# Kernel tuning notes

Hardware: AMD Instinct MI355X
Metric: run time of the kernel (lower is better)

## Reference

```python
import jax, jax.numpy as jnp
import numpy as np

# --- low precision float format: exp=5, man=2, subnormals, nearest-even ---
EXP, MAN = 5, 2
BIAS = 2 ** (EXP - 1) - 1          # 15
EMIN = 1 - BIAS                     # -14 (min normal exponent; clamping here gives subnormals)
MAXV = (2.0 - 2.0 ** (-MAN)) * 2.0 ** BIAS


def _q(x):
    """Round x to nearest FP(exp=5, man=2) value (subnormals, clipped at max)."""
    ax = jnp.abs(x)
    e = jnp.floor(jnp.log2(jnp.where(ax > 0, ax, 1.0)))
    e = jnp.maximum(e, EMIN)
    scale = jnp.exp2(e - MAN)
    q = jnp.round(x / scale) * scale   # jnp.round = half-to-even
    q = jnp.clip(q, -MAXV, MAXV)
    return jnp.where(ax > 0, q, x).astype(x.dtype)


# Quantizer: forward quantize, straight-through (quantized) backward
@jax.custom_vjp
def fq(x):
    return _q(x)

def _fq_fwd(x):
    return _q(x), None

def _fq_bwd(_, g):
    return (_q(g),)

fq.defvjp(_fq_fwd, _fq_bwd)


def conv_valid(x, w):
    return jax.lax.conv_general_dilated(
        x, w, window_strides=(1, 1), padding='VALID',
        dimension_numbers=('NCHW', 'OIHW', 'NCHW'))


def qconv(x, w):
    # QConv2d: input_quant, weight_quant, conv, output_quant
    return fq(conv_valid(fq(x), fq(w)))


def qlinear(x, W, b):
    # QLinear: input_quant, weight_quant (weights + bias), matmul, output_quant
    return fq(fq(x) @ fq(W).T + fq(b))


def batchnorm(x, gamma, beta, eps=1e-5):
    # training-mode BatchNorm2d over (N,H,W) per channel
    m = x.mean(axis=(0, 2, 3), keepdims=True)
    v = x.var(axis=(0, 2, 3), keepdims=True)
    return (x - m) * jax.lax.rsqrt(v + eps) * gamma[None, :, None, None] + beta[None, :, None, None]


def maxpool2(x):
    return jax.lax.reduce_window(x, -jnp.inf, jax.lax.max,
                                 (1, 1, 2, 2), (1, 1, 2, 2), 'VALID')


def setup_inputs() -> dict:
    key = jax.random.key(0)
    ks = jax.random.split(key, 12)
    B = 8192
    inp = {
        'x':   jax.random.normal(ks[0], (B, 1, 32, 32), jnp.float32),
        'w1':  jax.random.normal(ks[1], (6, 1, 5, 5), jnp.float32) * 0.2,
        'g1':  jnp.ones((6,), jnp.float32),
        'be1': jnp.zeros((6,), jnp.float32),
        'w2':  jax.random.normal(ks[2], (16, 6, 5, 5), jnp.float32) * 0.1,
        'g2':  jnp.ones((16,), jnp.float32),
        'be2': jnp.zeros((16,), jnp.float32),
        'fw1': jax.random.normal(ks[3], (120, 400), jnp.float32) * 0.05,
        'fb1': jnp.zeros((120,), jnp.float32),
        'fw2': jax.random.normal(ks[4], (84, 120), jnp.float32) * 0.09,
        'fb2': jnp.zeros((84,), jnp.float32),
        'fw3': jax.random.normal(ks[5], (10, 84), jnp.float32) * 0.1,
        'fb3': jnp.zeros((10,), jnp.float32),
    }
    return inp


def reference(x, w1, g1, be1, w2, g2, be2, fw1, fb1, fw2, fb2, fw3, fb3):
    x = fq(x)                                   # act_error_quant
    x = qconv(x, w1)                            # conv1 (no bias)
    x = batchnorm(x, g1, be1)                   # bn1
    x = fq(x)                                   # act_error_quant
    x = maxpool2(jax.nn.relu(x))                # relu + 2x2 maxpool -> [B,6,14,14]
    x = qconv(x, w2)                            # conv2 -> [B,16,10,10]
    x = batchnorm(x, g2, be2)                   # bn2
    x = fq(x)
    x = maxpool2(jax.nn.relu(x))                # -> [B,16,5,5]
    x = x.reshape(x.shape[0], -1)               # [B,400]
    x = jax.nn.relu(qlinear(x, fw1, fb1))       # fc1
    x = jax.nn.relu(qlinear(x, fw2, fb2))       # fc2
    x = qlinear(x, fw3, fb3)                    # fc3 -> [B,10]
    return x
```

## Files before the change

kernel.cpp:

```cpp
#include <hip/hip_runtime.h>
#include <hip/hip_bf16.h>


#define BATCH 8192

typedef double d4 __attribute__((ext_vector_type(4)));

__device__ __forceinline__ double fq_d(double x) {
    long long b = __double_as_longlong(x);
    long long ab = b & 0x7fffffffffffffffLL;
    if (ab == 0) return x;
    double q;
    if (ab >= 0x3F10000000000000LL) {
        long long r = b + 0x0001FFFFFFFFFFFFLL + ((b >> 50) & 1LL);
        r &= 0xFFFC000000000000LL;
        q = __longlong_as_double(r);
        q = fmin(fmax(q, -57344.0), 57344.0);
    } else {
        q = rint(x * 65536.0) * 1.52587890625e-05;
    }
    return q;
}

__device__ __forceinline__ float fq_f(float x) {
    int b = __float_as_int(x);
    int ab = b & 0x7fffffff;
    if (ab == 0) return x;
    float q;
    if (ab >= 0x38800000) {
        int r = b + 0x000FFFFF + ((b >> 21) & 1);
        r &= 0xFFE00000;
        q = __int_as_float(r);
        q = fminf(fmaxf(q, -57344.0f), 57344.0f);
    } else {
        q = rintf(x * 65536.0f) * 1.52587890625e-05f;
    }
    return q;
}

__device__ __forceinline__ unsigned short bfbits(double q) {
    __hip_bfloat16 h = __float2bfloat16((float)q);
    return *(unsigned short*)&h;
}

__global__ void kprep(const float* __restrict__ w1, const float* __restrict__ w2,
                      const float* __restrict__ fb1, const float* __restrict__ fb2,
                      const float* __restrict__ fb3, const float* __restrict__ fw1,
                      const float* __restrict__ fw2, const float* __restrict__ fw3,
                      float* __restrict__ qw1, float* __restrict__ qw2,
                      float* __restrict__ qfb1, float* __restrict__ qfb2,
                      float* __restrict__ qfb3, float* __restrict__ Wt1,
                      float* __restrict__ Wt2, float* __restrict__ Wt3) {
    int i = blockIdx.x * 256 + threadIdx.x;
    if (i < 150) { qw1[i] = fq_f(w1[i]); return; }
    i -= 150;
    if (i < 2400) { qw2[i] = fq_f(w2[i]); return; }
    i -= 2400;
    if (i < 120) { qfb1[i] = fq_f(fb1[i]); return; }
    i -= 120;
    if (i < 84) { qfb2[i] = fq_f(fb2[i]); return; }
    i -= 84;
    if (i < 10) { qfb3[i] = fq_f(fb3[i]); return; }
    i -= 10;
    if (i < 51200) { int k = i / 128, o = i % 128;
        Wt1[i] = (o < 120) ? fq_f(fw1[o * 400 + k]) : 0.0f; return; }
    i -= 51200;
    if (i < 15360) { int k = i / 128, o = i % 128;
        Wt2[i] = (o < 84) ? fq_f(fw2[o * 120 + k]) : 0.0f; return; }
    i -= 15360;
    if (i < 1344) { int k = i / 16, o = i % 16;
        Wt3[i] = (o < 10) ? fq_f(fw3[o * 84 + k]) : 0.0f; return; }
}
#define PREP_TOTAL (150 + 2400 + 120 + 84 + 10 + 51200 + 15360 + 1344)

__global__ __launch_bounds__(256) void kconv1(const float* __restrict__ x,
        const float* __restrict__ qw, __hip_bfloat16* __restrict__ c1,
        int nimg_total, double* __restrict__ st1) {
    __shared__ float sxf[3 * 1056];
    __shared__ double swd[152];
    __shared__ double sred[6][2];
    int t = threadIdx.x;
    int b0 = blockIdx.x * 3;
    int nimg = nimg_total - b0; if (nimg > 3) nimg = 3;
    for (int i = t; i < nimg * 1024; i += 256) {
        int img = i >> 10, idx = i & 1023;
        sxf[img * 1056 + (idx >> 5) * 33 + (idx & 31)] =
            fq_f(x[(size_t)(b0 + img) * 1024 + idx]);
    }
    if (t < 150) swd[t] = (double)qw[t];
    if (t >= 192 && t < 204) ((double*)sred)[t - 192] = 0.0;
    __syncthreads();
    int ntask = nimg * 336;
    for (int task = t; task < ntask; task += 256) {
        int img = task / 336; int rr = task % 336;
        int co = rr / 56; int rem = rr % 56;
        int i0 = (rem >> 2) * 2;
        int j0 = (rem & 3) * 7;
        const double* wp = &swd[co * 25];
        double a0[7], a1[7];
        #pragma unroll
        for (int j = 0; j < 7; ++j) { a0[j] = 0.0; a1[j] = 0.0; }
        double wr[5], wq[5];
        #pragma unroll
        for (int u = 0; u < 6; ++u) {
            const float* xr = &sxf[img * 1056 + (i0 + u) * 33 + j0];
            double xv[11];
            #pragma unroll
            for (int k = 0; k < 11; ++k) xv[k] = (double)xr[k];
            if (u < 5) {
                #pragma unroll
                for (int tt = 0; tt < 5; ++tt) wr[tt] = wp[u * 5 + tt];
                #pragma unroll
                for (int j = 0; j < 7; ++j)
                    a0[j] = fma(xv[j], wr[0], fma(xv[j+1], wr[1], fma(xv[j+2], wr[2],
                            fma(xv[j+3], wr[3], fma(xv[j+4], wr[4], a0[j])))));
            }
            if (u >= 1) {
                #pragma unroll
                for (int j = 0; j < 7; ++j)
                    a1[j] = fma(xv[j], wq[0], fma(xv[j+1], wq[1], fma(xv[j+2], wq[2],
                            fma(xv[j+3], wq[3], fma(xv[j+4], wq[4], a1[j])))));
            }
            #pragma unroll
            for (int tt = 0; tt < 5; ++tt) wq[tt] = wr[tt];
        }
        size_t base = ((size_t)(b0 + img) * 6 + co) * 784 + (size_t)i0 * 28 + j0;
        double s = 0.0, s2 = 0.0;
        #pragma unroll
        for (int j = 0; j < 7; ++j) {
            double q0 = fq_d(a0[j]), q1 = fq_d(a1[j]);
            ((unsigned short*)c1)[base + j]      = bfbits(q0);
            ((unsigned short*)c1)[base + 28 + j] = bfbits(q1);
            s += q0 + q1; s2 += q0 * q0 + q1 * q1;
        }
        atomicAdd(&sred[co][0], s);
        atomicAdd(&sred[co][1], s2);
    }
    __syncthreads();
    if (t < 12) atomicAdd(&st1[t * 32 + (blockIdx.x & 31)], ((double*)sred)[t]);
}

__global__ void kfinal(const double* __restrict__ st, double* __restrict__ mr,
                       int C, double N) {
    int c = threadIdx.x;
    if (c < C) {
        double s = 0.0, s2 = 0.0;
        for (int b = 0; b < 32; ++b) { s += st[c * 64 + b]; s2 += st[c * 64 + 32 + b]; }
        double m = s / N;
        double v = s2 / N - m * m;
        mr[2 * c] = m;
        mr[2 * c + 1] = 1.0 / sqrt(v + 1e-5);
    }
}

__global__ __launch_bounds__(256) void kpool1(const __hip_bfloat16* __restrict__ c1,
        const double* __restrict__ mr1, const float* __restrict__ g1,
        const float* __restrict__ be1, __hip_bfloat16* __restrict__ p1) {
    int idx = blockIdx.x * 256 + threadIdx.x;
    int pp = idx % 7;  int t1 = idx / 7;
    int ph = t1 % 14;  int t2 = t1 / 14;
    int c  = t2 % 6;   int b  = t2 / 6;
    double m = mr1[2 * c], r = mr1[2 * c + 1];
    double gg = (double)g1[c], bb = (double)be1[c];
    bool useMax = (r * gg) >= 0.0;
    const __hip_bfloat16* src = c1 + (((size_t)b * 6 + c) * 28 + 2 * ph) * 28 + 4 * pp;
    ushort4 u0 = *(const ushort4*)src;
    ushort4 u1 = *(const ushort4*)(src + 28);
    float f0 = __bfloat162float(*(__hip_bfloat16*)&u0.x), f1 = __bfloat162float(*(__hip_bfloat16*)&u0.y);
    float f2 = __bfloat162float(*(__hip_bfloat16*)&u0.z), f3 = __bfloat162float(*(__hip_bfloat16*)&u0.w);
    float f4 = __bfloat162float(*(__hip_bfloat16*)&u1.x), f5 = __bfloat162float(*(__hip_bfloat16*)&u1.y);
    float f6 = __bfloat162float(*(__hip_bfloat16*)&u1.z), f7 = __bfloat162float(*(__hip_bfloat16*)&u1.w);
    float va = useMax ? fmaxf(fmaxf(f0, f1), fmaxf(f4, f5))
                      : fminf(fminf(f0, f1), fminf(f4, f5));
    float vb = useMax ? fmaxf(fmaxf(f2, f3), fmaxf(f6, f7))
                      : fminf(fminf(f2, f3), fminf(f6, f7));
    double qa = fq_d((((double)va - m) * r) * gg + bb);
    double qb = fq_d((((double)vb - m) * r) * gg + bb);
    qa = fmax(qa, 0.0); qb = fmax(qb, 0.0);
    ushort2 pk; pk.x = bfbits(qa); pk.y = bfbits(qb);
    *(ushort2*)&p1[((size_t)b * 6 + c) * 196 + ph * 14 + 2 * pp] = pk;
}

__global__ __launch_bounds__(320) void kconv2(const __hip_bfloat16* __restrict__ p1,
        const float* __restrict__ qw, __hip_bfloat16* __restrict__ c2,
        double* __restrict__ st2) {
    __shared__ float sxf[9408];
    __shared__ double swd[2432];
    __shared__ int soff[152];
    __shared__ double sred[16][2];
    int t = threadIdx.x;
    int b0 = blockIdx.x * 8;
    const ushort4* srcp = (const ushort4*)(p1 + (size_t)b0 * 1176);
    for (int i = t; i < 2352; i += 320) {
        ushort4 u = srcp[i];
        float* d = &sxf[4 * i];
        d[0] = __bfloat162float(*(__hip_bfloat16*)&u.x);
        d[1] = __bfloat162float(*(__hip_bfloat16*)&u.y);
        d[2] = __bfloat162float(*(__hip_bfloat16*)&u.z);
        d[3] = __bfloat162float(*(__hip_bfloat16*)&u.w);
    }
    for (int i = t; i < 2432; i += 320) {
        int k = i >> 4, co = i & 15;
        swd[i] = (k < 150) ? (double)qw[co * 150 + k] : 0.0;
    }
    if (t < 152) {
        int k = t;
        soff[k] = (k < 150) ? (k / 25) * 196 + ((k % 25) / 5) * 14 + (k % 5) : 0;
    }
    if (t < 32) ((double*)sred)[t] = 0.0;
    __syncthreads();

    int l = t & 63, w = t >> 6;
    int c = l >> 4, r16 = l & 15;

    d4 pz = {0.0, 0.0, 0.0, 0.0};
    d4 prow = __builtin_amdgcn_mfma_f64_16x16x4f64((double)r16, 0.25, pz, 0, 0, 0);
    d4 pcol = __builtin_amdgcn_mfma_f64_16x16x4f64(1.0, 0.25 * (double)r16, pz, 0, 0, 0);
    int rowidx[4], colidx[4];
    #pragma unroll
    for (int j = 0; j < 4; ++j) { rowidx[j] = (int)prow[j]; colidx[j] = (int)pcol[j]; }

    double bw[38];
    #pragma unroll
    for (int s = 0; s < 38; ++s) bw[s] = swd[(4 * s + c) * 16 + r16];

    double ls = 0.0, ls2 = 0.0;
    int co0 = colidx[0];
    for (int tile = w; tile < 50; tile += 5) {
        int pos = tile * 16 + r16;
        int img = pos / 100, pp = pos % 100;
        int abase = img * 1176 + (pp / 10) * 14 + (pp % 10);
        d4 acc = {0.0, 0.0, 0.0, 0.0};
        #pragma unroll
        for (int s = 0; s < 38; ++s) {
            double av = (double)sxf[abase + soff[4 * s + c]];
            acc = __builtin_amdgcn_mfma_f64_16x16x4f64(av, bw[s], acc, 0, 0, 0);
        }
        #pragma unroll
        for (int j = 0; j < 4; ++j) {
            int po = tile * 16 + rowidx[j];
            int im2 = po / 100, pq = po % 100;
            double q = fq_d(acc[j]);
            ((unsigned short*)c2)[((size_t)(b0 + im2) * 100 + pq) * 16 + colidx[j]] = bfbits(q);
            ls += q; ls2 += q * q;
        }
    }
    atomicAdd(&sred[co0][0], ls);
    atomicAdd(&sred[co0][1], ls2);
    __syncthreads();
    if (t < 32) atomicAdd(&st2[t * 32 + (blockIdx.x & 31)], ((double*)sred)[t]);
}

__global__ __launch_bounds__(256) void kfc1(const __hip_bfloat16* __restrict__ c2,
        const double* __restrict__ st2, const float* __restrict__ g2,
        const float* __restrict__ be2, const float* __restrict__ Wt,
        const float* __restrict__ qb, __hip_bfloat16* __restrict__ outb) {
    constexpr int IN = 400, OUT = 120, OUTP = 128, ROWS = 4, BT = 8;
    __shared__ double sx[BT][IN];
    __shared__ double sbn[16][4];
    int t = threadIdx.x;
    int b0 = blockIdx.x * BT;
    if (t < 16) {
        double s = 0.0, s2 = 0.0;
        for (int b = 0; b < 32; ++b) { s += st2[t * 64 + b]; s2 += st2[t * 64 + 32 + b]; }
        double m = s / (819200.0);
        double v = s2 / (819200.0) - m * m;
        sbn[t][0] = m; sbn[t][1] = 1.0 / sqrt(v + 1e-5);
        sbn[t][2] = (double)g2[t]; sbn[t][3] = (double)be2[t];
    }
    __syncthreads();
    for (int i = t; i < BT * IN; i += 256) {
        int r = i / IN, k = i % IN;
        int c = k / 25, rem = k % 25;
        int ph = rem / 5, pw = rem % 5;
        const __hip_bfloat16* src = c2 + ((size_t)(b0 + r) * 100 + 20 * ph + 2 * pw) * 16 + c;
        double m = sbn[c][0], rr = sbn[c][1], gg = sbn[c][2], bb = sbn[c][3];
        float f0 = __bfloat162float(src[0]),   f1 = __bfloat162float(src[16]);
        float f2 = __bfloat162float(src[160]), f3 = __bfloat162float(src[176]);
        bool useMax = (rr * gg) >= 0.0;
        float v = useMax ? fmaxf(fmaxf(f0, f1), fmaxf(f2, f3))
                         : fminf(fminf(f0, f1), fminf(f2, f3));
        double q = fq_d((((double)v - m) * rr) * gg + bb);
        sx[r][k] = fmax(q, 0.0);
    }
    __syncthreads();
    int o = t % OUTP;
    int g = t / OUTP;
    double acc[ROWS];
    double bias = (o < OUT) ? (double)qb[o] : 0.0;
    #pragma unroll
    for (int r = 0; r < ROWS; ++r) acc[r] = bias;
    #pragma unroll 4
    for (int k = 0; k < IN; ++k) {
        double w = (double)Wt[k * OUTP + o];
        #pragma unroll
        for (int r = 0; r < ROWS; ++r)
            acc[r] = fma(sx[g * ROWS + r][k], w, acc[r]);
    }
    if (o < OUT) {
        #pragma unroll
        for (int r = 0; r < ROWS; ++r) {
            double q = fq_d(acc[r]);
            if (q < 0.0) q = 0.0;
            outb[(size_t)(b0 + g * ROWS + r) * OUT + o] = __float2bfloat16((float)q);
        }
    }
}

__global__ __launch_bounds__(256) void kfc23(const __hip_bfloat16* __restrict__ a1,
        const float* __restrict__ Wt2, const float* __restrict__ qfb2,
        const float* __restrict__ Wt3, const float* __restrict__ qfb3,
        float* __restrict__ out) {
    __shared__ double sx1[16][120];
    __shared__ double s2[16][84];
    int t = threadIdx.x;
    int b0 = blockIdx.x * 16;
    for (int i = t; i < 16 * 120; i += 256) {
        int r = i / 120, k = i % 120;
        sx1[r][k] = (double)__bfloat162float(a1[(size_t)(b0 + r) * 120 + k]);
    }
    __syncthreads();
    {
        int o = t % 128, g = t / 128;
        double acc[8];
        double bias = (o < 84) ? (double)qfb2[o] : 0.0;
        #pragma unroll
        for (int r = 0; r < 8; ++r) acc[r] = bias;
        #pragma unroll 4
        for (int k = 0; k < 120; ++k) {
            double w = (double)Wt2[k * 128 + o];
            #pragma unroll
            for (int r = 0; r < 8; ++r)
                acc[r] = fma(sx1[g * 8 + r][k], w, acc[r]);
        }
        if (o < 84) {
            #pragma unroll
            for (int r = 0; r < 8; ++r) {
                double q = fq_d(acc[r]);
                s2[g * 8 + r][o] = fmax(q, 0.0);
            }
        }
    }
    __syncthreads();
    {
        int o = t % 16, g = t / 16;
        double acc = (o < 10) ? (double)qfb3[o] : 0.0;
        #pragma unroll 4
        for (int k = 0; k < 84; ++k)
            acc = fma(s2[g][k], (double)Wt3[k * 16 + o], acc);
        if (o < 10)
            out[(size_t)(b0 + g) * 10 + o] = (float)fq_d(acc);
    }
}

extern "C" void kernel_launch(void* const* d_in, const int* in_sizes, int n_in,
                              void* d_out, int out_size, void* d_ws, size_t ws_size,
                              hipStream_t stream) {
    const float* x   = (const float*)d_in[0];
    const float* w1  = (const float*)d_in[1];
    const float* g1  = (const float*)d_in[2];
    const float* be1 = (const float*)d_in[3];
    const float* w2  = (const float*)d_in[4];
    const float* g2  = (const float*)d_in[5];
    const float* be2 = (const float*)d_in[6];
    const float* fw1 = (const float*)d_in[7];
    const float* fb1 = (const float*)d_in[8];
    const float* fw2 = (const float*)d_in[9];
    const float* fb2 = (const float*)d_in[10];
    const float* fw3 = (const float*)d_in[11];
    const float* fb3 = (const float*)d_in[12];

    char* ws = (char*)d_ws;
    double* stats1 = (double*)(ws + 0);
    double* stats2 = (double*)(ws + 3072);
    double* mr1    = (double*)(ws + 11264);
    float* qw1  = (float*)(ws + 12288);
    float* qw2  = (float*)(ws + 13312);
    float* qfb1 = (float*)(ws + 23040);
    float* qfb2 = (float*)(ws + 23552);
    float* qfb3 = (float*)(ws + 24064);
    float* Wt1  = (float*)(ws + 24576);
    float* Wt2  = (float*)(ws + 229376);
    float* Wt3  = (float*)(ws + 290816);
    __hip_bfloat16* c1 = (__hip_bfloat16*)(ws + 303104);
    __hip_bfloat16* p1 = (__hip_bfloat16*)(ws + 77373440);
    __hip_bfloat16* c2 = (__hip_bfloat16*)(ws + 303104);
    __hip_bfloat16* a1 = (__hip_bfloat16*)(ws + 303104 + 26214400);

    hipMemsetAsync(ws, 0, 11264, stream);

    kprep<<<(PREP_TOTAL + 255) / 256, 256, 0, stream>>>(
        w1, w2, fb1, fb2, fb3, fw1, fw2, fw3,
        qw1, qw2, qfb1, qfb2, qfb3, Wt1, Wt2, Wt3);

    kconv1<<<(BATCH + 2) / 3, 256, 0, stream>>>(x, qw1, c1, BATCH, stats1);
    kfinal<<<1, 32, 0, stream>>>(stats1, mr1, 6, (double)BATCH * 784.0);
    kpool1<<<BATCH * 6 * 14 * 7 / 256, 256, 0, stream>>>(c1, mr1, g1, be1, p1);
    kconv2<<<BATCH / 8, 320, 0, stream>>>(p1, qw2, c2, stats2);
    kfc1<<<BATCH / 8, 256, 0, stream>>>(c2, stats2, g2, be2, Wt1, qfb1, a1);
    kfc23<<<BATCH / 16, 256, 0, stream>>>(a1, Wt2, qfb2, Wt3, qfb3, (float*)d_out);
}
```

Baseline: 437.1 us.

## Shrink conv2 blocks, drop register-held weights, and coalesce fc1 pooled loads

The conv2 kernel now handles 4 images per 256-thread block instead of 8 per 320 threads. Weights stay in LDS as floats rather than being preloaded into a 38-double register array, and patch offsets are computed arithmetically instead of read from an LDS table. Each lane group takes a contiguous k range split over two independent MFMA accumulators, which cuts VGPR pressure and LDS footprint to allow 4 blocks per CU while adding ILP. The extra LDS weight loads and index arithmetic per MFMA may cost issue slots. Separately, fc1's pooling loop now puts the channel index in the fastest-varying thread dimension, so reads from the channel-last conv2 output coalesce.

New measurement: 535.1 us. 1.22x slower.

```diff
diff --git a/kernel.cpp b/kernel.cpp
--- a/kernel.cpp
+++ b/kernel.cpp
@@ -41,6 +41,18 @@
 __device__ __forceinline__ unsigned short bfbits(double q) {
     __hip_bfloat16 h = __float2bfloat16((float)q);
     return *(unsigned short*)&h;
+}
+
+__device__ __forceinline__ float bfval(unsigned short u) {
+    return __bfloat162float(*(__hip_bfloat16*)&u);
+}
+
+__device__ __forceinline__ int patch_off(int k) {
+    int ci = (k * 1311) >> 15;
+    int rem = k - 25 * ci;
+    int u = (rem * 13) >> 6;
+    int v = rem - 5 * u;
+    return ci * 196 + u * 14 + v;
 }
 
 __global__ void kprep(const float* __restrict__ w1, const float* __restrict__ w2,
@@ -166,10 +178,10 @@
     const __hip_bfloat16* src = c1 + (((size_t)b * 6 + c) * 28 + 2 * ph) * 28 + 4 * pp;
     ushort4 u0 = *(const ushort4*)src;
     ushort4 u1 = *(const ushort4*)(src + 28);
-    float f0 = __bfloat162float(*(__hip_bfloat16*)&u0.x), f1 = __bfloat162float(*(__hip_bfloat16*)&u0.y);
-    float f2 = __bfloat162float(*(__hip_bfloat16*)&u0.z), f3 = __bfloat162float(*(__hip_bfloat16*)&u0.w);
-    float f4 = __bfloat162float(*(__hip_bfloat16*)&u1.x), f5 = __bfloat162float(*(__hip_bfloat16*)&u1.y);
-    float f6 = __bfloat162float(*(__hip_bfloat16*)&u1.z), f7 = __bfloat162float(*(__hip_bfloat16*)&u1.w);
+    float f0 = bfval(u0.x), f1 = bfval(u0.y);
+    float f2 = bfval(u0.z), f3 = bfval(u0.w);
+    float f4 = bfval(u1.x), f5 = bfval(u1.y);
+    float f6 = bfval(u1.z), f7 = bfval(u1.w);
     float va = useMax ? fmaxf(fmaxf(f0, f1), fmaxf(f4, f5))
                       : fminf(fminf(f0, f1), fminf(f4, f5));
     float vb = useMax ? fmaxf(fmaxf(f2, f3), fmaxf(f6, f7))
@@ -181,31 +193,26 @@
     *(ushort2*)&p1[((size_t)b * 6 + c) * 196 + ph * 14 + 2 * pp] = pk;
 }
 
-__global__ __launch_bounds__(320) void kconv2(const __hip_bfloat16* __restrict__ p1,
+__global__ __launch_bounds__(256, 4) void kconv2(const __hip_bfloat16* __restrict__ p1,
         const float* __restrict__ qw, __hip_bfloat16* __restrict__ c2,
         double* __restrict__ st2) {
-    __shared__ float sxf[9408];
-    __shared__ double swd[2432];
-    __shared__ int soff[152];
+    __shared__ float sxf[4704];
+    __shared__ float swf[2432];
     __shared__ double sred[16][2];
     int t = threadIdx.x;
-    int b0 = blockIdx.x * 8;
+    int b0 = blockIdx.x * 4;
     const ushort4* srcp = (const ushort4*)(p1 + (size_t)b0 * 1176);
-    for (int i = t; i < 2352; i += 320) {
+    for (int i = t; i < 1176; i += 256) {
         ushort4 u = srcp[i];
         float* d = &sxf[4 * i];
-        d[0] = __bfloat162float(*(__hip_bfloat16*)&u.x);
-        d[1] = __bfloat162float(*(__hip_bfloat16*)&u.y);
-        d[2] = __bfloat162float(*(__hip_bfloat16*)&u.z);
-        d[3] = __bfloat162float(*(__hip_bfloat16*)&u.w);
-    }
-    for (int i = t; i < 2432; i += 320) {
+        d[0] = bfval(u.x);
+        d[1] = bfval(u.y);
+        d[2] = bfval(u.z);
+        d[3] = bfval(u.w);
+    }
+    for (int i = t; i < 2432; i += 256) {
         int k = i >> 4, co = i & 15;
-        swd[i] = (k < 150) ? (double)qw[co * 150 + k] : 0.0;
-    }
-    if (t < 152) {
-        int k = t;
-        soff[k] = (k < 150) ? (k / 25) * 196 + ((k % 25) / 5) * 14 + (k % 5) : 0;
+        swf[i] = (k < 150) ? qw[co * 150 + k] : 0.0f;
     }
     if (t < 32) ((double*)sred)[t] = 0.0;
     __syncthreads();
@@ -220,28 +227,33 @@
     #pragma unroll
     for (int j = 0; j < 4; ++j) { rowidx[j] = (int)prow[j]; colidx[j] = (int)pcol[j]; }
 
-    double bw[38];
-    #pragma unroll
-    for (int s = 0; s < 38; ++s) bw[s] = swd[(4 * s + c) * 16 + r16];
-
+    int kbase = 38 * c;
     double ls = 0.0, ls2 = 0.0;
     int co0 = colidx[0];
-    for (int tile = w; tile < 50; tile += 5) {
+    for (int tile = w; tile < 25; tile += 4) {
         int pos = tile * 16 + r16;
-        int img = pos / 100, pp = pos % 100;
-        int abase = img * 1176 + (pp / 10) * 14 + (pp % 10);
-        d4 acc = {0.0, 0.0, 0.0, 0.0};
-        #pragma unroll
-        for (int s = 0; s < 38; ++s) {
-            double av = (double)sxf[abase + soff[4 * s + c]];
-            acc = __builtin_amdgcn_mfma_f64_16x16x4f64(av, bw[s], acc, 0, 0, 0);
+        int abase = (pos / 100) * 1176 + ((pos % 100) / 10) * 14 + (pos % 10);
+        d4 a0 = {0.0, 0.0, 0.0, 0.0}, a1 = {0.0, 0.0, 0.0, 0.0};
+        #pragma unroll
+        for (int s = 0; s < 19; ++s) {
+            int k0 = kbase + s;
+            int k1 = kbase + s + 19;
+            int i0 = abase + patch_off(k0);
+            int i1 = abase + patch_off(k1);
+            if (i0 > 4703) i0 = 0;
+            if (i1 > 4703) i1 = 0;
+            double x0 = (double)sxf[i0];
+            double x1 = (double)sxf[i1];
+            double w0 = (double)swf[k0 * 16 + r16];
+            double w1 = (double)swf[k1 * 16 + r16];
+            a0 = __builtin_amdgcn_mfma_f64_16x16x4f64(x0, w0, a0, 0, 0, 0);
+            a1 = __builtin_amdgcn_mfma_f64_16x16x4f64(x1, w1, a1, 0, 0, 0);
         }
         #pragma unroll
         for (int j = 0; j < 4; ++j) {
+            double q = fq_d(a0[j] + a1[j]);
             int po = tile * 16 + rowidx[j];
-            int im2 = po / 100, pq = po % 100;
-            double q = fq_d(acc[j]);
-            ((unsigned short*)c2)[((size_t)(b0 + im2) * 100 + pq) * 16 + colidx[j]] = bfbits(q);
+            ((unsigned short*)c2)[((size_t)(b0 + po / 100) * 100 + po % 100) * 16 + colidx[j]] = bfbits(q);
             ls += q; ls2 += q * q;
         }
     }
@@ -270,18 +282,19 @@
     }
     __syncthreads();
     for (int i = t; i < BT * IN; i += 256) {
-        int r = i / IN, k = i % IN;
-        int c = k / 25, rem = k % 25;
+        int cc = i & 15;
+        int rem = (i >> 4) % 25;
+        int r = i / 400;
         int ph = rem / 5, pw = rem % 5;
-        const __hip_bfloat16* src = c2 + ((size_t)(b0 + r) * 100 + 20 * ph + 2 * pw) * 16 + c;
-        double m = sbn[c][0], rr = sbn[c][1], gg = sbn[c][2], bb = sbn[c][3];
+        const __hip_bfloat16* src = c2 + ((size_t)(b0 + r) * 100 + 20 * ph + 2 * pw) * 16 + cc;
+        double m = sbn[cc][0], rr = sbn[cc][1], gg = sbn[cc][2], bb = sbn[cc][3];
         float f0 = __bfloat162float(src[0]),   f1 = __bfloat162float(src[16]);
         float f2 = __bfloat162float(src[160]), f3 = __bfloat162float(src[176]);
         bool useMax = (rr * gg) >= 0.0;
         float v = useMax ? fmaxf(fmaxf(f0, f1), fmaxf(f2, f3))
                          : fminf(fminf(f0, f1), fminf(f2, f3));
         double q = fq_d((((double)v - m) * rr) * gg + bb);
-        sx[r][k] = fmax(q, 0.0);
+        sx[r][cc * 25 + rem] = fmax(q, 0.0);
     }
     __syncthreads();
     int o = t % OUTP;
@@ -396,7 +409,7 @@
     kconv1<<<(BATCH + 2) / 3, 256, 0, stream>>>(x, qw1, c1, BATCH, stats1);
     kfinal<<<1, 32, 0, stream>>>(stats1, mr1, 6, (double)BATCH * 784.0);
     kpool1<<<BATCH * 6 * 14 * 7 / 256, 256, 0, stream>>>(c1, mr1, g1, be1, p1);
-    kconv2<<<BATCH / 8, 320, 0, stream>>>(p1, qw2, c2, stats2);
+    kconv2<<<BATCH / 4, 256, 0, stream>>>(p1, qw2, c2, stats2);
     kfc1<<<BATCH / 8, 256, 0, stream>>>(c2, stats2, g2, be2, Wt1, qfb1, a1);
     kfc23<<<BATCH / 16, 256, 0, stream>>>(a1, Wt2, qfb2, Wt3, qfb3, (float*)d_out);
 }
```
